# Kernel tuning notes

Measured on AMD Instinct MI355X. Metric: run time of the kernel, lower is better.

Reference implementation:

```python
import jax, jax.numpy as jnp
import numpy as np

N = 20000   # nodes
K = 32      # neighbors per node (kNN graph)
C = 128     # input feature dim
H = 256     # h_theta hidden/output dim
E = N * K   # edges


def setup_inputs() -> dict:
    key = jax.random.key(0)
    k1, k2, k3, k4 = jax.random.split(key, 4)
    node_features = jax.random.normal(k1, (N, C), dtype=jnp.float32)
    senders = jax.random.randint(k2, (E,), 0, N)              # neighbor node per edge
    receivers = jnp.repeat(jnp.arange(N), K)                  # center node per edge (k-NN: exactly K each)
    W1 = jax.random.normal(k3, (2 * C, H), dtype=jnp.float32) * (1.0 / np.sqrt(2 * C))
    b1 = jnp.zeros((H,), dtype=jnp.float32)
    W2 = jax.random.normal(k4, (H, H), dtype=jnp.float32) * (1.0 / np.sqrt(H))
    b2 = jnp.zeros((H,), dtype=jnp.float32)
    return {"node_features": node_features, "senders": senders, "receivers": receivers,
            "W1": W1, "b1": b1, "W2": W2, "b2": b2}


def reference(node_features, senders, receivers, W1, b1, W2, b2):
    # gather: x_v (center) and x_vp (neighbor) per edge -> [E, C]
    x_v = node_features[receivers]
    x_vp = node_features[senders]
    # edge feature: concat([x_v, x_vp - x_v]) -> [E, 2C]
    e = jnp.concatenate([x_v, x_vp - x_v], axis=-1)
    # h_theta MLP per edge -> [E, H]
    h = jnp.dot(jax.nn.relu(jnp.dot(e, W1) + b1), W2) + b2
    # max-reduce over each node's incident edges -> [N, H]
    return jax.ops.segment_max(h, receivers, num_segments=N)
```

## Files before the change

### kernel.cpp

```cpp
#include <hip/hip_runtime.h>
#include <hip/hip_bf16.h>

#define NN    20000
#define KNN   32
#define CIN   128
#define HD    256
#define EE    (NN * KNN)
#define MT    64
#define TPB   10
#define NBLK  (EE / (MT * TPB))

typedef __bf16 bf16x8_t __attribute__((ext_vector_type(8)));
typedef __bf16 bf16x4_t __attribute__((ext_vector_type(4)));
typedef float  f32x4_t  __attribute__((ext_vector_type(4)));

__device__ __forceinline__ void gload_lds16(const __bf16* g, __bf16* l) {
    __builtin_amdgcn_global_load_lds(
        (const __attribute__((address_space(1))) void*)g,
        (__attribute__((address_space(3))) void*)l, 16, 0, 0);
}

__global__ void ec_prep(const float* __restrict__ nf, const float* __restrict__ W1,
                        const float* __restrict__ W2, __bf16* __restrict__ nfb,
                        __bf16* __restrict__ w1g, __bf16* __restrict__ w2t) {
    int bid = blockIdx.x;
    if (bid < (NN * CIN) / 1024) {
        int i = (bid * 256 + threadIdx.x) * 4;
        float4 v = *(const float4*)(nf + i);
        bf16x4_t b = { (__bf16)v.x, (__bf16)v.y, (__bf16)v.z, (__bf16)v.w };
        *(bf16x4_t*)(nfb + i) = b;
    } else {
        int idx = (bid - (NN * CIN) / 1024) * 256 + threadIdx.x;
        int k = idx >> 8, n = idx & 255;
        float v = (k < CIN) ? (W1[k * 256 + n] - W1[(k + CIN) * 256 + n])
                            : W1[k * 256 + n];
        int kt = k >> 5, qr = (k >> 3) & 3, j = k & 7;
        w1g[(size_t)((kt * 4 + qr) * 256 + n) * 8 + j] = (__bf16)v;
        w2t[n * 256 + k] = (__bf16)W2[k * 256 + n];
    }
}

__global__ __launch_bounds__(512, 2) void ec_main(
    const __bf16* __restrict__ nfb,
    const int*   __restrict__ senders,
    const __bf16* __restrict__ w1g,
    const __bf16* __restrict__ w2t,
    const float* __restrict__ b1,
    const float* __restrict__ b2,
    float* __restrict__ out)
{
    __shared__ __attribute__((aligned(16))) __bf16 ldsE[2][8192];
    __shared__ __attribute__((aligned(16))) __bf16 ldsH[2][16384];
    __shared__ __attribute__((aligned(16))) float  ldsY[20 * 256];

    const int tid  = threadIdx.x;
    const int lane = tid & 63;
    const int wave = tid >> 6;
    const int qrow = lane >> 4;
    const int lcol = lane & 15;
    const int blk  = blockIdx.x;
    const int fsl  = wave * 32;
    const int fs2  = (wave >> 1) * 64;
    const int eh   = wave & 1;
    const int p0 = wave * 2, p1 = wave * 2 + 1;
    const int c0 = p0 >> 2, q0 = p0 & 3;
    const int c1 = p1 >> 2, q1 = p1 & 3;

    int sidxAll[TPB];
#pragma unroll
    for (int tt = 0; tt < TPB; ++tt)
        sidxAll[tt] = senders[(blk * TPB + tt) * MT + lane];

    gload_lds16(nfb + (size_t)sidxAll[0] * CIN + c0 * 32 + q0 * 8, &ldsE[0][p0 * 512]);
    gload_lds16(nfb + (size_t)sidxAll[0] * CIN + c1 * 32 + q1 * 8, &ldsE[0][p1 * 512]);

    {
        f32x4_t ay[2][2];
#pragma unroll
        for (int mi = 0; mi < 2; ++mi)
#pragma unroll
            for (int ni = 0; ni < 2; ++ni)
                ay[mi][ni] = (f32x4_t){0.f, 0.f, 0.f, 0.f};
        bf16x8_t xv[2][4];
#pragma unroll
        for (int ni = 0; ni < 2; ++ni) {
            int ln = ni * 16 + lcol; if (ln > 19) ln = 19;
            const __bf16* row = nfb + (size_t)(blk * 20 + ln) * CIN;
#pragma unroll
            for (int c = 0; c < 4; ++c)
                xv[ni][c] = *(const bf16x8_t*)(row + c * 32 + qrow * 8);
        }
#pragma unroll
        for (int kt = 0; kt < 4; ++kt) {
            bf16x8_t wy[2];
#pragma unroll
            for (int mi = 0; mi < 2; ++mi)
                wy[mi] = *(const bf16x8_t*)(w1g +
                    (size_t)((kt * 4 + qrow) * 256 + fsl + mi * 16 + lcol) * 8);
#pragma unroll
            for (int mi = 0; mi < 2; ++mi)
#pragma unroll
                for (int ni = 0; ni < 2; ++ni)
                    ay[mi][ni] = __builtin_amdgcn_mfma_f32_16x16x32_bf16(
                        wy[mi], xv[ni][kt], ay[mi][ni], 0, 0, 0);
        }
#pragma unroll
        for (int mi = 0; mi < 2; ++mi)
#pragma unroll
            for (int ni = 0; ni < 2; ++ni) {
                int ln = ni * 16 + lcol;
                if (ln < 20)
                    *(f32x4_t*)(ldsY + ln * 256 + fsl + mi * 16 + qrow * 4) = ay[mi][ni];
            }
    }

    bf16x8_t w2f[8][4];
#pragma unroll
    for (int kt = 0; kt < 8; ++kt)
#pragma unroll
        for (int ni = 0; ni < 4; ++ni)
            w2f[kt][ni] = *(const bf16x8_t*)(w2t + (size_t)(fs2 + ni * 16 + lcol) * 256
                                                 + kt * 32 + qrow * 8);

    float4 bias1[2];
#pragma unroll
    for (int mi = 0; mi < 2; ++mi)
        bias1[mi] = *(const float4*)(b1 + fsl + mi * 16 + qrow * 4);
    float bias2[4];
#pragma unroll
    for (int ni = 0; ni < 4; ++ni)
        bias2[ni] = b2[fs2 + ni * 16 + lcol];

    const __bf16* w1b = w1g + 32768;

    __syncthreads();

#pragma unroll 1
    for (int t = 0; t < TPB; ++t) {
        const int node0 = (blk * TPB + t) * 2;
        const int cur = t & 1;

        if (t + 1 < TPB) {
            const __bf16* srow = nfb + (size_t)sidxAll[t + 1] * CIN;
            gload_lds16(srow + c0 * 32 + q0 * 8, &ldsE[1 - cur][p0 * 512]);
            gload_lds16(srow + c1 * 32 + q1 * 8, &ldsE[1 - cur][p1 * 512]);
        }

        f32x4_t acc[2][4];
#pragma unroll
        for (int mi = 0; mi < 2; ++mi)
#pragma unroll
            for (int ni = 0; ni < 4; ++ni)
                acc[mi][ni] = *(const f32x4_t*)(ldsY + (t * 2 + (ni >> 1)) * 256
                                                + fsl + mi * 16 + qrow * 4);
#pragma unroll
        for (int kt = 0; kt < 4; ++kt) {
            bf16x8_t wf[2], ef[4];
#pragma unroll
            for (int mi = 0; mi < 2; ++mi)
                wf[mi] = *(const bf16x8_t*)(w1b +
                    (size_t)((kt * 4 + qrow) * 256 + fsl + mi * 16 + lcol) * 8);
#pragma unroll
            for (int ni = 0; ni < 4; ++ni)
                ef[ni] = *(const bf16x8_t*)(&ldsE[cur][0] +
                    (size_t)((kt * 4 + qrow) * 64 + ni * 16 + lcol) * 8);
#pragma unroll
            for (int mi = 0; mi < 2; ++mi)
#pragma unroll
                for (int ni = 0; ni < 4; ++ni)
                    acc[mi][ni] = __builtin_amdgcn_mfma_f32_16x16x32_bf16(
                        wf[mi], ef[ni], acc[mi][ni], 0, 0, 0);
        }

#pragma unroll
        for (int mi = 0; mi < 2; ++mi) {
            const int f0  = fsl + mi * 16 + qrow * 4;
            const int ktp = f0 >> 5, qrp = (f0 >> 3) & 3, jh = f0 & 7;
            float4 bb = bias1[mi];
#pragma unroll
            for (int ni = 0; ni < 4; ++ni) {
                int edge = ni * 16 + lcol;
                float v0 = acc[mi][ni][0] + bb.x;
                float v1 = acc[mi][ni][1] + bb.y;
                float v2 = acc[mi][ni][2] + bb.z;
                float v3 = acc[mi][ni][3] + bb.w;
                bf16x4_t h = { (__bf16)fmaxf(v0, 0.f), (__bf16)fmaxf(v1, 0.f),
                               (__bf16)fmaxf(v2, 0.f), (__bf16)fmaxf(v3, 0.f) };
                *(bf16x4_t*)(&ldsH[cur][0] + (size_t)((ktp * 4 + qrp) * 64 + edge) * 8 + jh) = h;
            }
        }

        __syncthreads();

        f32x4_t acc2[2][4];
#pragma unroll
        for (int mi = 0; mi < 2; ++mi)
#pragma unroll
            for (int ni = 0; ni < 4; ++ni)
                acc2[mi][ni] = (f32x4_t){0.f, 0.f, 0.f, 0.f};
#pragma unroll
        for (int kt = 0; kt < 8; ++kt) {
            bf16x8_t af[2];
#pragma unroll
            for (int mi = 0; mi < 2; ++mi)
                af[mi] = *(const bf16x8_t*)(&ldsH[cur][0] +
                    (size_t)((kt * 4 + qrow) * 64 + eh * 32 + mi * 16 + lcol) * 8);
#pragma unroll
            for (int mi = 0; mi < 2; ++mi)
#pragma unroll
                for (int ni = 0; ni < 4; ++ni)
                    acc2[mi][ni] = __builtin_amdgcn_mfma_f32_16x16x32_bf16(
                        af[mi], w2f[kt][ni], acc2[mi][ni], 0, 0, 0);
        }

#pragma unroll
        for (int ni = 0; ni < 4; ++ni) {
            int col = fs2 + ni * 16 + lcol;
            float mx = -3.402823466e38f;
#pragma unroll
            for (int mi = 0; mi < 2; ++mi)
#pragma unroll
                for (int r = 0; r < 4; ++r)
                    mx = fmaxf(mx, acc2[mi][ni][r]);
            mx = fmaxf(mx, __shfl_xor(mx, 16, 64));
            mx = fmaxf(mx, __shfl_xor(mx, 32, 64));
            if (qrow == 0)
                out[(size_t)(node0 + eh) * HD + col] = mx + bias2[ni];
        }
    }
}

extern "C" void kernel_launch(void* const* d_in, const int* in_sizes, int n_in,
                              void* d_out, int out_size, void* d_ws, size_t ws_size,
                              hipStream_t stream) {
    const float* nf      = (const float*)d_in[0];
    const int*   senders = (const int*)d_in[1];
    const float* W1 = (const float*)d_in[3];
    const float* b1 = (const float*)d_in[4];
    const float* W2 = (const float*)d_in[5];
    const float* b2 = (const float*)d_in[6];

    __bf16* w1g = (__bf16*)d_ws;
    __bf16* w2t = w1g + 256 * 256;
    __bf16* nfb = w2t + 256 * 256;

    ec_prep<<<(NN * CIN) / 1024 + 256, 256, 0, stream>>>(nf, W1, W2, nfb, w1g, w2t);
    ec_main<<<NBLK, 512, 0, stream>>>(nfb, senders, w1g, w2t, b1, b2, (float*)d_out);
}
```

Before: 221.7 us.

## Process one node per iteration with 32-edge tiles and higher occupancy

The main loop now handles one node (32 edges) per iteration instead of two nodes (64 edges), and each wave owns a 32-column slice for both GEMMs. This halves the LDS buffers and the W2 fragments held in registers, which allows launch bounds of 4 blocks per SM. Sender indices are prefetched one step ahead instead of all at the start. The trade-off is twice as many iterations and barriers per block, and fewer MFMAs per barrier, in exchange for more resident waves to hide gather latency.

```diff
diff --git a/kernel.cpp b/kernel.cpp
--- a/kernel.cpp
+++ b/kernel.cpp
@@ -6,9 +6,8 @@
 #define CIN   128
 #define HD    256
 #define EE    (NN * KNN)
-#define MT    64
-#define TPB   10
-#define NBLK  (EE / (MT * TPB))
+#define NT    20
+#define NBLK  (NN / NT)
 
 typedef __bf16 bf16x8_t __attribute__((ext_vector_type(8)));
 typedef __bf16 bf16x4_t __attribute__((ext_vector_type(4)));
@@ -40,7 +39,7 @@
     }
 }
 
-__global__ __launch_bounds__(512, 2) void ec_main(
+__global__ __launch_bounds__(512, 4) void ec_main(
     const __bf16* __restrict__ nfb,
     const int*   __restrict__ senders,
     const __bf16* __restrict__ w1g,
@@ -49,9 +48,9 @@
     const float* __restrict__ b2,
     float* __restrict__ out)
 {
-    __shared__ __attribute__((aligned(16))) __bf16 ldsE[2][8192];
-    __shared__ __attribute__((aligned(16))) __bf16 ldsH[2][16384];
-    __shared__ __attribute__((aligned(16))) float  ldsY[20 * 256];
+    __shared__ __attribute__((aligned(16))) __bf16 ldsE[2][4096];
+    __shared__ __attribute__((aligned(16))) __bf16 ldsH[2][8192];
+    __shared__ __attribute__((aligned(16))) float  ldsY[NT * 256];
 
     const int tid  = threadIdx.x;
     const int lane = tid & 63;
@@ -60,19 +59,15 @@
     const int lcol = lane & 15;
     const int blk  = blockIdx.x;
     const int fsl  = wave * 32;
-    const int fs2  = (wave >> 1) * 64;
-    const int eh   = wave & 1;
-    const int p0 = wave * 2, p1 = wave * 2 + 1;
-    const int c0 = p0 >> 2, q0 = p0 & 3;
-    const int c1 = p1 >> 2, q1 = p1 & 3;
-
-    int sidxAll[TPB];
-#pragma unroll
-    for (int tt = 0; tt < TPB; ++tt)
-        sidxAll[tt] = senders[(blk * TPB + tt) * MT + lane];
-
-    gload_lds16(nfb + (size_t)sidxAll[0] * CIN + c0 * 32 + q0 * 8, &ldsE[0][p0 * 512]);
-    gload_lds16(nfb + (size_t)sidxAll[0] * CIN + c1 * 32 + q1 * 8, &ldsE[0][p1 * 512]);
+    const int e5   = lane & 31;
+    const int ch   = wave * 2 + (lane >> 5);
+    const int soff = (ch >> 2) * 32 + (ch & 3) * 8;
+
+    {
+        int s0 = senders[(blk * NT) * KNN + e5];
+        gload_lds16(nfb + (size_t)s0 * CIN + soff, &ldsE[0][wave * 512]);
+    }
+    int sn = senders[(blk * NT + 1) * KNN + e5];
 
     {
         f32x4_t ay[2][2];
@@ -84,8 +79,8 @@
         bf16x8_t xv[2][4];
 #pragma unroll
         for (int ni = 0; ni < 2; ++ni) {
-            int ln = ni * 16 + lcol; if (ln > 19) ln = 19;
-            const __bf16* row = nfb + (size_t)(blk * 20 + ln) * CIN;
+            int ln = ni * 16 + lcol; if (ln > NT - 1) ln = NT - 1;
+            const __bf16* row = nfb + (size_t)(blk * NT + ln) * CIN;
 #pragma unroll
             for (int c = 0; c < 4; ++c)
                 xv[ni][c] = *(const bf16x8_t*)(row + c * 32 + qrow * 8);
@@ -109,76 +104,75 @@
 #pragma unroll
             for (int ni = 0; ni < 2; ++ni) {
                 int ln = ni * 16 + lcol;
-                if (ln < 20)
+                if (ln < NT)
                     *(f32x4_t*)(ldsY + ln * 256 + fsl + mi * 16 + qrow * 4) = ay[mi][ni];
             }
     }
 
-    bf16x8_t w2f[8][4];
+    bf16x8_t w2f[8][2];
 #pragma unroll
     for (int kt = 0; kt < 8; ++kt)
 #pragma unroll
-        for (int ni = 0; ni < 4; ++ni)
-            w2f[kt][ni] = *(const bf16x8_t*)(w2t + (size_t)(fs2 + ni * 16 + lcol) * 256
+        for (int ni = 0; ni < 2; ++ni)
+            w2f[kt][ni] = *(const bf16x8_t*)(w2t + (size_t)(fsl + ni * 16 + lcol) * 256
                                                  + kt * 32 + qrow * 8);
 
     float4 bias1[2];
 #pragma unroll
     for (int mi = 0; mi < 2; ++mi)
         bias1[mi] = *(const float4*)(b1 + fsl + mi * 16 + qrow * 4);
-    float bias2[4];
-#pragma unroll
-    for (int ni = 0; ni < 4; ++ni)
-        bias2[ni] = b2[fs2 + ni * 16 + lcol];
+    float bias2[2];
+#pragma unroll
+    for (int ni = 0; ni < 2; ++ni)
+        bias2[ni] = b2[fsl + ni * 16 + lcol];
 
     const __bf16* w1b = w1g + 32768;
 
     __syncthreads();
 
 #pragma unroll 1
-    for (int t = 0; t < TPB; ++t) {
-        const int node0 = (blk * TPB + t) * 2;
+    for (int t = 0; t < NT; ++t) {
         const int cur = t & 1;
 
-        if (t + 1 < TPB) {
-            const __bf16* srow = nfb + (size_t)sidxAll[t + 1] * CIN;
-            gload_lds16(srow + c0 * 32 + q0 * 8, &ldsE[1 - cur][p0 * 512]);
-            gload_lds16(srow + c1 * 32 + q1 * 8, &ldsE[1 - cur][p1 * 512]);
-        }
-
-        f32x4_t acc[2][4];
-#pragma unroll
-        for (int mi = 0; mi < 2; ++mi)
-#pragma unroll
-            for (int ni = 0; ni < 4; ++ni)
-                acc[mi][ni] = *(const f32x4_t*)(ldsY + (t * 2 + (ni >> 1)) * 256
-                                                + fsl + mi * 16 + qrow * 4);
+        int sn2 = sn;
+        if (t + 2 < NT) sn2 = senders[(blk * NT + t + 2) * KNN + e5];
+
+        if (t + 1 < NT)
+            gload_lds16(nfb + (size_t)sn * CIN + soff, &ldsE[1 - cur][wave * 512]);
+
+        f32x4_t acc[2][2];
+#pragma unroll
+        for (int mi = 0; mi < 2; ++mi) {
+            f32x4_t y = *(const f32x4_t*)(ldsY + t * 256 + fsl + mi * 16 + qrow * 4);
+            acc[mi][0] = y;
+            acc[mi][1] = y;
+        }
 #pragma unroll
         for (int kt = 0; kt < 4; ++kt) {
-            bf16x8_t wf[2], ef[4];
+            bf16x8_t wf[2], ef[2];
 #pragma unroll
             for (int mi = 0; mi < 2; ++mi)
                 wf[mi] = *(const bf16x8_t*)(w1b +
                     (size_t)((kt * 4 + qrow) * 256 + fsl + mi * 16 + lcol) * 8);
 #pragma unroll
-            for (int ni = 0; ni < 4; ++ni)
+            for (int ni = 0; ni < 2; ++ni)
                 ef[ni] = *(const bf16x8_t*)(&ldsE[cur][0] +
-                    (size_t)((kt * 4 + qrow) * 64 + ni * 16 + lcol) * 8);
-#pragma unroll
-            for (int mi = 0; mi < 2; ++mi)
-#pragma unroll
-                for (int ni = 0; ni < 4; ++ni)
+                    (size_t)((kt * 4 + qrow) * 32 + ni * 16 + lcol) * 8);
+#pragma unroll
+            for (int mi = 0; mi < 2; ++mi)
+#pragma unroll
+                for (int ni = 0; ni < 2; ++ni)
                     acc[mi][ni] = __builtin_amdgcn_mfma_f32_16x16x32_bf16(
                         wf[mi], ef[ni], acc[mi][ni], 0, 0, 0);
         }
 
 #pragma unroll
         for (int mi = 0; mi < 2; ++mi) {
-            const int f0  = fsl + mi * 16 + qrow * 4;
-            const int ktp = f0 >> 5, qrp = (f0 >> 3) & 3, jh = f0 & 7;
+            const int f0 = fsl + mi * 16 + qrow * 4;
+            const int cq = f0 >> 3, jh = f0 & 7;
             float4 bb = bias1[mi];
 #pragma unroll
-            for (int ni = 0; ni < 4; ++ni) {
+            for (int ni = 0; ni < 2; ++ni) {
                 int edge = ni * 16 + lcol;
                 float v0 = acc[mi][ni][0] + bb.x;
                 float v1 = acc[mi][ni][1] + bb.y;
@@ -186,36 +180,35 @@
                 float v3 = acc[mi][ni][3] + bb.w;
                 bf16x4_t h = { (__bf16)fmaxf(v0, 0.f), (__bf16)fmaxf(v1, 0.f),
                                (__bf16)fmaxf(v2, 0.f), (__bf16)fmaxf(v3, 0.f) };
-                *(bf16x4_t*)(&ldsH[cur][0] + (size_t)((ktp * 4 + qrp) * 64 + edge) * 8 + jh) = h;
+                *(bf16x4_t*)(&ldsH[cur][0] + (size_t)(cq * 32 + edge) * 8 + jh) = h;
             }
         }
 
         __syncthreads();
 
-        f32x4_t acc2[2][4];
+        f32x4_t acc2[2][2];
 #pragma unroll
         for (int mi = 0; mi < 2; ++mi)
 #pragma unroll
-            for (int ni = 0; ni < 4; ++ni)
+            for (int ni = 0; ni < 2; ++ni)
                 acc2[mi][ni] = (f32x4_t){0.f, 0.f, 0.f, 0.f};
 #pragma unroll
-        for (int kt = 0; kt < 8; ++kt) {
+        for (int kt2 = 0; kt2 < 8; ++kt2) {
             bf16x8_t af[2];
 #pragma unroll
             for (int mi = 0; mi < 2; ++mi)
                 af[mi] = *(const bf16x8_t*)(&ldsH[cur][0] +
-                    (size_t)((kt * 4 + qrow) * 64 + eh * 32 + mi * 16 + lcol) * 8);
-#pragma unroll
-            for (int mi = 0; mi < 2; ++mi)
-#pragma unroll
-                for (int ni = 0; ni < 4; ++ni)
+                    (size_t)((kt2 * 4 + qrow) * 32 + mi * 16 + lcol) * 8);
+#pragma unroll
+            for (int mi = 0; mi < 2; ++mi)
+#pragma unroll
+                for (int ni = 0; ni < 2; ++ni)
                     acc2[mi][ni] = __builtin_amdgcn_mfma_f32_16x16x32_bf16(
-                        af[mi], w2f[kt][ni], acc2[mi][ni], 0, 0, 0);
-        }
-
-#pragma unroll
-        for (int ni = 0; ni < 4; ++ni) {
-            int col = fs2 + ni * 16 + lcol;
+                        af[mi], w2f[kt2][ni], acc2[mi][ni], 0, 0, 0);
+        }
+
+#pragma unroll
+        for (int ni = 0; ni < 2; ++ni) {
             float mx = -3.402823466e38f;
 #pragma unroll
             for (int mi = 0; mi < 2; ++mi)
@@ -225,8 +218,10 @@
             mx = fmaxf(mx, __shfl_xor(mx, 16, 64));
             mx = fmaxf(mx, __shfl_xor(mx, 32, 64));
             if (qrow == 0)
-                out[(size_t)(node0 + eh) * HD + col] = mx + bias2[ni];
-        }
+                out[(size_t)(blk * NT + t) * HD + fsl + ni * 16 + lcol] = mx + bias2[ni];
+        }
+
+        sn = sn2;
     }
 }
 
```

After: 247.3 us. 11.5% more time.

## Precompute per-node first-layer projections and gather projected rows per edge

Applied to the files above, without the earlier changes.

The first linear layer is split algebraically into per-node terms. A new kernel computes, once per node, the center contribution plus bias (P, fp32) and the neighbor contribution (Z, bf16). The main kernel then gathers Z rows by sender and adds P before the ReLU, so the per-edge first-layer GEMM is gone. The cost is an extra kernel launch, a workspace round-trip of about 20k×256 values in each of P and Z, wider per-edge gathers (256 bf16 instead of 128), and occupancy lowered to one block per CU.

```diff
diff --git a/kernel.cpp b/kernel.cpp
--- a/kernel.cpp
+++ b/kernel.cpp
@@ -6,19 +6,12 @@
 #define CIN   128
 #define HD    256
 #define EE    (NN * KNN)
-#define MT    64
-#define TPB   10
-#define NBLK  (EE / (MT * TPB))
+#define NT    10
+#define NBLK  (NN / (2 * NT))
 
 typedef __bf16 bf16x8_t __attribute__((ext_vector_type(8)));
 typedef __bf16 bf16x4_t __attribute__((ext_vector_type(4)));
 typedef float  f32x4_t  __attribute__((ext_vector_type(4)));
-
-__device__ __forceinline__ void gload_lds16(const __bf16* g, __bf16* l) {
-    __builtin_amdgcn_global_load_lds(
-        (const __attribute__((address_space(1))) void*)g,
-        (__attribute__((address_space(3))) void*)l, 16, 0, 0);
-}
 
 __global__ void ec_prep(const float* __restrict__ nf, const float* __restrict__ W1,
                         const float* __restrict__ W2, __bf16* __restrict__ nfb,
@@ -40,18 +33,126 @@
     }
 }
 
-__global__ __launch_bounds__(512, 2) void ec_main(
-    const __bf16* __restrict__ nfb,
+__global__ __launch_bounds__(512, 1) void ec_pz(
+    const __bf16* __restrict__ nfb, const __bf16* __restrict__ w1g,
+    const float* __restrict__ b1, float* __restrict__ Pq, __bf16* __restrict__ Zq)
+{
+    __shared__ __attribute__((aligned(16))) float ldsT[32 * 256];
+
+    const int tid  = threadIdx.x;
+    const int lane = tid & 63;
+    const int wave = tid >> 6;
+    const int qrow = lane >> 4;
+    const int lcol = lane & 15;
+    const int blk  = blockIdx.x;
+    const int fsl  = wave * 32;
+
+    bf16x8_t xv[2][4];
+#pragma unroll
+    for (int ni = 0; ni < 2; ++ni) {
+        const __bf16* row = nfb + (size_t)(blk * 32 + ni * 16 + lcol) * CIN;
+#pragma unroll
+        for (int c = 0; c < 4; ++c)
+            xv[ni][c] = *(const bf16x8_t*)(row + c * 32 + qrow * 8);
+    }
+
+    float4 bias1[2];
+#pragma unroll
+    for (int mi = 0; mi < 2; ++mi)
+        bias1[mi] = *(const float4*)(b1 + fsl + mi * 16 + qrow * 4);
+
+    {
+        f32x4_t ay[2][2];
+#pragma unroll
+        for (int mi = 0; mi < 2; ++mi)
+#pragma unroll
+            for (int ni = 0; ni < 2; ++ni)
+                ay[mi][ni] = (f32x4_t){0.f, 0.f, 0.f, 0.f};
+#pragma unroll
+        for (int kt = 0; kt < 4; ++kt) {
+            bf16x8_t wy[2];
+#pragma unroll
+            for (int mi = 0; mi < 2; ++mi)
+                wy[mi] = *(const bf16x8_t*)(w1g +
+                    (size_t)((kt * 4 + qrow) * 256 + fsl + mi * 16 + lcol) * 8);
+#pragma unroll
+            for (int mi = 0; mi < 2; ++mi)
+#pragma unroll
+                for (int ni = 0; ni < 2; ++ni)
+                    ay[mi][ni] = __builtin_amdgcn_mfma_f32_16x16x32_bf16(
+                        wy[mi], xv[ni][kt], ay[mi][ni], 0, 0, 0);
+        }
+#pragma unroll
+        for (int mi = 0; mi < 2; ++mi)
+#pragma unroll
+            for (int ni = 0; ni < 2; ++ni) {
+                f32x4_t v = ay[mi][ni];
+                v[0] += bias1[mi].x; v[1] += bias1[mi].y;
+                v[2] += bias1[mi].z; v[3] += bias1[mi].w;
+                *(f32x4_t*)(ldsT + (ni * 16 + lcol) * 256 + fsl + mi * 16 + qrow * 4) = v;
+            }
+    }
+    __syncthreads();
+    {
+        float4* dst = (float4*)(Pq + (size_t)blk * 32 * 256);
+        const float4* src = (const float4*)ldsT;
+#pragma unroll
+        for (int i = 0; i < 4; ++i)
+            dst[tid * 4 + i] = src[tid * 4 + i];
+    }
+    __syncthreads();
+
+    {
+        f32x4_t az[2][2];
+#pragma unroll
+        for (int mi = 0; mi < 2; ++mi)
+#pragma unroll
+            for (int ni = 0; ni < 2; ++ni)
+                az[mi][ni] = (f32x4_t){0.f, 0.f, 0.f, 0.f};
+#pragma unroll
+        for (int kt = 0; kt < 4; ++kt) {
+            bf16x8_t wy[2];
+#pragma unroll
+            for (int mi = 0; mi < 2; ++mi)
+                wy[mi] = *(const bf16x8_t*)(w1g +
+                    (size_t)((16 + kt * 4 + qrow) * 256 + fsl + mi * 16 + lcol) * 8);
+#pragma unroll
+            for (int mi = 0; mi < 2; ++mi)
+#pragma unroll
+                for (int ni = 0; ni < 2; ++ni)
+                    az[mi][ni] = __builtin_amdgcn_mfma_f32_16x16x32_bf16(
+                        wy[mi], xv[ni][kt], az[mi][ni], 0, 0, 0);
+        }
+#pragma unroll
+        for (int mi = 0; mi < 2; ++mi)
+#pragma unroll
+            for (int ni = 0; ni < 2; ++ni)
+                *(f32x4_t*)(ldsT + (ni * 16 + lcol) * 256 + fsl + mi * 16 + qrow * 4)
+                    = az[mi][ni];
+    }
+    __syncthreads();
+    {
+        const float4* src = (const float4*)ldsT;
+        __bf16* dst = Zq + (size_t)blk * 32 * 256;
+#pragma unroll
+        for (int i = 0; i < 4; ++i) {
+            float4 v = src[tid * 4 + i];
+            bf16x4_t b = { (__bf16)v.x, (__bf16)v.y, (__bf16)v.z, (__bf16)v.w };
+            *(bf16x4_t*)(dst + (size_t)(tid * 4 + i) * 4) = b;
+        }
+    }
+}
+
+__global__ __launch_bounds__(512, 1) void ec_main(
+    const __bf16* __restrict__ Zq,
     const int*   __restrict__ senders,
-    const __bf16* __restrict__ w1g,
+    const float* __restrict__ Pq,
     const __bf16* __restrict__ w2t,
-    const float* __restrict__ b1,
     const float* __restrict__ b2,
     float* __restrict__ out)
 {
-    __shared__ __attribute__((aligned(16))) __bf16 ldsE[2][8192];
     __shared__ __attribute__((aligned(16))) __bf16 ldsH[2][16384];
-    __shared__ __attribute__((aligned(16))) float  ldsY[20 * 256];
+    __shared__ __attribute__((aligned(16))) float  ldsP[20 * 256];
 
     const int tid  = threadIdx.x;
     const int lane = tid & 63;
@@ -62,56 +163,17 @@
     const int fsl  = wave * 32;
     const int fs2  = (wave >> 1) * 64;
     const int eh   = wave & 1;
-    const int p0 = wave * 2, p1 = wave * 2 + 1;
-    const int c0 = p0 >> 2, q0 = p0 & 3;
-    const int c1 = p1 >> 2, q1 = p1 & 3;
-
-    int sidxAll[TPB];
-#pragma unroll
-    for (int tt = 0; tt < TPB; ++tt)
-        sidxAll[tt] = senders[(blk * TPB + tt) * MT + lane];
-
-    gload_lds16(nfb + (size_t)sidxAll[0] * CIN + c0 * 32 + q0 * 8, &ldsE[0][p0 * 512]);
-    gload_lds16(nfb + (size_t)sidxAll[0] * CIN + c1 * 32 + q1 * 8, &ldsE[0][p1 * 512]);
-
-    {
-        f32x4_t ay[2][2];
-#pragma unroll
-        for (int mi = 0; mi < 2; ++mi)
-#pragma unroll
-            for (int ni = 0; ni < 2; ++ni)
-                ay[mi][ni] = (f32x4_t){0.f, 0.f, 0.f, 0.f};
-        bf16x8_t xv[2][4];
-#pragma unroll
-        for (int ni = 0; ni < 2; ++ni) {
-            int ln = ni * 16 + lcol; if (ln > 19) ln = 19;
-            const __bf16* row = nfb + (size_t)(blk * 20 + ln) * CIN;
-#pragma unroll
-            for (int c = 0; c < 4; ++c)
-                xv[ni][c] = *(const bf16x8_t*)(row + c * 32 + qrow * 8);
-        }
-#pragma unroll
-        for (int kt = 0; kt < 4; ++kt) {
-            bf16x8_t wy[2];
-#pragma unroll
-            for (int mi = 0; mi < 2; ++mi)
-                wy[mi] = *(const bf16x8_t*)(w1g +
-                    (size_t)((kt * 4 + qrow) * 256 + fsl + mi * 16 + lcol) * 8);
-#pragma unroll
-            for (int mi = 0; mi < 2; ++mi)
-#pragma unroll
-                for (int ni = 0; ni < 2; ++ni)
-                    ay[mi][ni] = __builtin_amdgcn_mfma_f32_16x16x32_bf16(
-                        wy[mi], xv[ni][kt], ay[mi][ni], 0, 0, 0);
-        }
-#pragma unroll
-        for (int mi = 0; mi < 2; ++mi)
-#pragma unroll
-            for (int ni = 0; ni < 2; ++ni) {
-                int ln = ni * 16 + lcol;
-                if (ln < 20)
-                    *(f32x4_t*)(ldsY + ln * 256 + fsl + mi * 16 + qrow * 4) = ay[mi][ni];
-            }
+
+    int sidxAll[NT];
+#pragma unroll
+    for (int tt = 0; tt < NT; ++tt)
+        sidxAll[tt] = senders[(blk * NT + tt) * 64 + lane];
+
+    {
+        const float4* src = (const float4*)(Pq + (size_t)blk * 20 * 256);
+        float4* dst = (float4*)ldsP;
+        for (int i = tid; i < 1280; i += 512)
+            dst[i] = src[i];
     }
 
     bf16x8_t w2f[8][4];
@@ -121,76 +183,45 @@
         for (int ni = 0; ni < 4; ++ni)
             w2f[kt][ni] = *(const bf16x8_t*)(w2t + (size_t)(fs2 + ni * 16 + lcol) * 256
                                                  + kt * 32 + qrow * 8);
-
-    float4 bias1[2];
-#pragma unroll
-    for (int mi = 0; mi < 2; ++mi)
-        bias1[mi] = *(const float4*)(b1 + fsl + mi * 16 + qrow * 4);
     float bias2[4];
 #pragma unroll
     for (int ni = 0; ni < 4; ++ni)
         bias2[ni] = b2[fs2 + ni * 16 + lcol];
 
-    const __bf16* w1b = w1g + 32768;
-
+    bf16x8_t zf[4];
+#pragma unroll
+    for (int c = 0; c < 4; ++c)
+        zf[c] = *(const bf16x8_t*)(Zq + (size_t)sidxAll[0] * HD + fsl + c * 8);
+
+    __syncthreads();
+
+    {
+        const int nl = 0 * 2 + (lane >> 5);
+        const float* pf = ldsP + nl * 256 + fsl;
+#pragma unroll
+        for (int c = 0; c < 4; ++c) {
+            f32x4_t p0 = *(const f32x4_t*)(pf + c * 8);
+            f32x4_t p1 = *(const f32x4_t*)(pf + c * 8 + 4);
+            bf16x8_t h;
+#pragma unroll
+            for (int j = 0; j < 4; ++j) {
+                h[j]     = (__bf16)fmaxf(p0[j] + (float)zf[c][j], 0.f);
+                h[j + 4] = (__bf16)fmaxf(p1[j] + (float)zf[c][j + 4], 0.f);
+            }
+            *(bf16x8_t*)(&ldsH[0][0] + (size_t)((wave * 4 + c) * 64 + lane) * 8) = h;
+        }
+    }
     __syncthreads();
 
 #pragma unroll 1
-    for (int t = 0; t < TPB; ++t) {
-        const int node0 = (blk * TPB + t) * 2;
+    for (int t = 0; t < NT; ++t) {
         const int cur = t & 1;
 
-        if (t + 1 < TPB) {
-            const __bf16* srow = nfb + (size_t)sidxAll[t + 1] * CIN;
-            gload_lds16(srow + c0 * 32 + q0 * 8, &ldsE[1 - cur][p0 * 512]);
-            gload_lds16(srow + c1 * 32 + q1 * 8, &ldsE[1 - cur][p1 * 512]);
-        }
-
-        f32x4_t acc[2][4];
-#pragma unroll
-        for (int mi = 0; mi < 2; ++mi)
-#pragma unroll
-            for (int ni = 0; ni < 4; ++ni)
-                acc[mi][ni] = *(const f32x4_t*)(ldsY + (t * 2 + (ni >> 1)) * 256
-                                                + fsl + mi * 16 + qrow * 4);
-#pragma unroll
-        for (int kt = 0; kt < 4; ++kt) {
-            bf16x8_t wf[2], ef[4];
-#pragma unroll
-            for (int mi = 0; mi < 2; ++mi)
-                wf[mi] = *(const bf16x8_t*)(w1b +
-                    (size_t)((kt * 4 + qrow) * 256 + fsl + mi * 16 + lcol) * 8);
-#pragma unroll
-            for (int ni = 0; ni < 4; ++ni)
-                ef[ni] = *(const bf16x8_t*)(&ldsE[cur][0] +
-                    (size_t)((kt * 4 + qrow) * 64 + ni * 16 + lcol) * 8);
-#pragma unroll
-            for (int mi = 0; mi < 2; ++mi)
-#pragma unroll
-                for (int ni = 0; ni < 4; ++ni)
-                    acc[mi][ni] = __builtin_amdgcn_mfma_f32_16x16x32_bf16(
-                        wf[mi], ef[ni], acc[mi][ni], 0, 0, 0);
-        }
-
-#pragma unroll
-        for (int mi = 0; mi < 2; ++mi) {
-            const int f0  = fsl + mi * 16 + qrow * 4;
-            const int ktp = f0 >> 5, qrp = (f0 >> 3) & 3, jh = f0 & 7;
-            float4 bb = bias1[mi];
-#pragma unroll
-            for (int ni = 0; ni < 4; ++ni) {
-                int edge = ni * 16 + lcol;
-                float v0 = acc[mi][ni][0] + bb.x;
-                float v1 = acc[mi][ni][1] + bb.y;
-                float v2 = acc[mi][ni][2] + bb.z;
-                float v3 = acc[mi][ni][3] + bb.w;
-                bf16x4_t h = { (__bf16)fmaxf(v0, 0.f), (__bf16)fmaxf(v1, 0.f),
-                               (__bf16)fmaxf(v2, 0.f), (__bf16)fmaxf(v3, 0.f) };
-                *(bf16x4_t*)(&ldsH[cur][0] + (size_t)((ktp * 4 + qrp) * 64 + edge) * 8 + jh) = h;
-            }
-        }
-
-        __syncthreads();
+        if (t + 1 < NT) {
+#pragma unroll
+            for (int c = 0; c < 4; ++c)
+                zf[c] = *(const bf16x8_t*)(Zq + (size_t)sidxAll[t + 1] * HD + fsl + c * 8);
+        }
 
         f32x4_t acc2[2][4];
 #pragma unroll
@@ -215,7 +246,6 @@
 
 #pragma unroll
         for (int ni = 0; ni < 4; ++ni) {
-            int col = fs2 + ni * 16 + lcol;
             float mx = -3.402823466e38f;
 #pragma unroll
             for (int mi = 0; mi < 2; ++mi)
@@ -225,8 +255,28 @@
             mx = fmaxf(mx, __shfl_xor(mx, 16, 64));
             mx = fmaxf(mx, __shfl_xor(mx, 32, 64));
             if (qrow == 0)
-                out[(size_t)(node0 + eh) * HD + col] = mx + bias2[ni];
-        }
+                out[(size_t)((blk * NT + t) * 2 + eh) * HD + fs2 + ni * 16 + lcol]
+                    = mx + bias2[ni];
+        }
+
+        if (t + 1 < NT) {
+            const int nl = (t + 1) * 2 + (lane >> 5);
+            const float* pf = ldsP + nl * 256 + fsl;
+#pragma unroll
+            for (int c = 0; c < 4; ++c) {
+                f32x4_t p0 = *(const f32x4_t*)(pf + c * 8);
+                f32x4_t p1 = *(const f32x4_t*)(pf + c * 8 + 4);
+                bf16x8_t h;
+#pragma unroll
+                for (int j = 0; j < 4; ++j) {
+                    h[j]     = (__bf16)fmaxf(p0[j] + (float)zf[c][j], 0.f);
+                    h[j + 4] = (__bf16)fmaxf(p1[j] + (float)zf[c][j + 4], 0.f);
+                }
+                *(bf16x8_t*)(&ldsH[1 - cur][0] + (size_t)((wave * 4 + c) * 64 + lane) * 8) = h;
+            }
+        }
+
+        __syncthreads();
     }
 }
 
@@ -243,7 +293,10 @@
     __bf16* w1g = (__bf16*)d_ws;
     __bf16* w2t = w1g + 256 * 256;
     __bf16* nfb = w2t + 256 * 256;
+    __bf16* Zq  = nfb + (size_t)NN * CIN;
+    float*  Pq  = (float*)(Zq + (size_t)NN * HD);
 
     ec_prep<<<(NN * CIN) / 1024 + 256, 256, 0, stream>>>(nf, W1, W2, nfb, w1g, w2t);
-    ec_main<<<NBLK, 512, 0, stream>>>(nfb, senders, w1g, w2t, b1, b2, (float*)d_out);
+    ec_pz<<<NN / 32, 512, 0, stream>>>(nfb, w1g, b1, Pq, Zq);
+    ec_main<<<NBLK, 512, 0, stream>>>(Zq, senders, Pq, w2t, b2, (float*)d_out);
 }
```

Measured after the change: 220.9 us. No clear change (-0.4%).
